# Kernel tuning notes

Measured on AMD Instinct MI355X. Metric: run time of the kernel, lower is better.

## Reference

```python
import jax, jax.numpy as jnp
import numpy as np

S, B, E = 2048, 2, 1024   # seq, batch, hidden (transpose_batch_sequence=True -> [S,B,E])
H, D = 16, 64             # num_heads, head_dim; H*D == E
EPS = 1e-6


def setup_inputs() -> dict:
    key = jax.random.key(0)
    k1, k2, k3 = jax.random.split(key, 3)
    x = jax.random.normal(k1, (S, B, E), dtype=jnp.float32)
    ln_scale = jnp.ones((E,), dtype=jnp.float32)
    # variance-scaling fan_in init ~ N(0, 1/fan_in); query block scaled by 1/sqrt(head_dim)
    w_qkv = jax.random.normal(k2, (E, 3 * H * D), dtype=jnp.float32) / np.sqrt(E)
    w_qkv = w_qkv.at[:, : H * D].divide(np.sqrt(D))  # scaled_query_init
    w_out = jax.random.normal(k3, (H * D, E), dtype=jnp.float32) / np.sqrt(H * D)
    return {"x": x, "ln_scale": ln_scale, "w_qkv": w_qkv, "w_out": w_out}


def reference(x, ln_scale, w_qkv, w_out):
    # LayerNormDenseGeneral: layernorm (scale only) fused with QKV projection
    mu = jnp.mean(x, axis=-1, keepdims=True)
    var = jnp.mean(jnp.square(x - mu), axis=-1, keepdims=True)
    ln = (x - mu) * jax.lax.rsqrt(var + EPS) * ln_scale          # [S,B,E]
    qkv = jnp.einsum('sbe,ef->sbf', ln, w_qkv)                    # [S,B,3HD]
    q, k, v = jnp.split(qkv, 3, axis=-1)
    q = q.reshape(S, B, H, D)
    k = k.reshape(S, B, H, D)
    v = v.reshape(S, B, H, D)
    # core_attention (transpose_batch_sequence=True): full score matrix
    attn = jnp.einsum('qbhd,kbhd->bhqk', q, k)                    # [B,H,S,S]
    attn = jax.nn.softmax(attn, axis=-1)
    ctx = jnp.einsum('bhqk,kbhd->qbhd', attn, v)                  # [S,B,H,D]
    ctx = ctx.reshape(S, B, H * D)
    out = jnp.einsum('sbf,fe->sbe', ctx, w_out)                   # output projection
    return out
```

## Files before the change

### kernel.cpp

```cpp
#include <hip/hip_runtime.h>
#include <math.h>


typedef unsigned short u16;
typedef unsigned int u32;
typedef __bf16 bf16x8 __attribute__((ext_vector_type(8)));
typedef float f32x4 __attribute__((ext_vector_type(4)));
typedef u16 u16x8 __attribute__((ext_vector_type(8)));
typedef u16 u16x4 __attribute__((ext_vector_type(4)));
typedef u32 u32x2 __attribute__((ext_vector_type(2)));

#define S_LEN 2048
#define BATCH 2
#define EDIM  1024
#define NHEAD 16
#define DHEAD 64
#define MROWS 4096
#define NQKV  3072
#define KDIM  1024
#define LOG2E 1.4426950408889634f

__device__ __forceinline__ float bf2f(u16 u) {
  union { unsigned int u; float f; } v; v.u = ((unsigned int)u) << 16; return v.f;
}
__device__ __forceinline__ u16 f2bf(float f) {
  union { float f; unsigned int u; } v; v.f = f;
  return (u16)((v.u + 0x7FFFu + ((v.u >> 16) & 1u)) >> 16);
}
__device__ __forceinline__ u32 cvt_pk_bf16(float lo, float hi) {
  u32 r;
  asm("v_cvt_pk_bf16_f32 %0, %1, %2" : "=v"(r) : "v"(lo), "v"(hi));
  return r;
}
__device__ __forceinline__ void glds16(const void* g, void* l) {
  __builtin_amdgcn_global_load_lds((__attribute__((address_space(1))) void*)g,
                                   (__attribute__((address_space(3))) void*)l,
                                   16, 0, 0);
}

__global__ void detect_kernel(const u16* __restrict__ x, int* __restrict__ flag) {
  const int t = threadIdx.x;
  const u16 v = x[t];
  const int e = (v >> 7) & 0xFF;
  const int ok = (e >= 100 && e <= 140) ? 1 : 0;
  const unsigned long long m = __ballot(ok);
  if (t == 0) *flag = (__popcll(m) >= 56) ? 1 : 0;
}

__global__ __launch_bounds__(256) void ln_kernel(const void* __restrict__ xv,
                                                 const void* __restrict__ scv,
                                                 u16* __restrict__ out,
                                                 const int* __restrict__ flag) {
  const int row = blockIdx.x;
  const int t = threadIdx.x;
  const int isbf = *flag;
  float v0, v1, v2, v3;
  if (isbf) {
    u16x4 xin = *(const u16x4*)((const u16*)xv + (size_t)row * EDIM + t * 4);
    v0 = bf2f(xin[0]); v1 = bf2f(xin[1]); v2 = bf2f(xin[2]); v3 = bf2f(xin[3]);
  } else {
    float4 xin = *(const float4*)((const float*)xv + (size_t)row * EDIM + t * 4);
    v0 = xin.x; v1 = xin.y; v2 = xin.z; v3 = xin.w;
  }
  float s  = v0 + v1 + v2 + v3;
  float ss = v0 * v0 + v1 * v1 + v2 * v2 + v3 * v3;
  #pragma unroll
  for (int off = 1; off < 64; off <<= 1) {
    s  += __shfl_xor(s, off);
    ss += __shfl_xor(ss, off);
  }
  __shared__ float ps[4], pq[4];
  const int w = t >> 6;
  if ((t & 63) == 0) { ps[w] = s; pq[w] = ss; }
  __syncthreads();
  s  = ps[0] + ps[1] + ps[2] + ps[3];
  ss = pq[0] + pq[1] + pq[2] + pq[3];
  const float mu   = s * (1.0f / EDIM);
  const float rstd = rsqrtf(ss * (1.0f / EDIM) - mu * mu + 1e-6f);
  float sc0, sc1, sc2, sc3;
  if (isbf) {
    const u16* sc = (const u16*)scv + t * 4;
    sc0 = bf2f(sc[0]); sc1 = bf2f(sc[1]); sc2 = bf2f(sc[2]); sc3 = bf2f(sc[3]);
  } else {
    const float* sc = (const float*)scv + t * 4;
    sc0 = sc[0]; sc1 = sc[1]; sc2 = sc[2]; sc3 = sc[3];
  }
  u16x4 o;
  o[0] = f2bf((v0 - mu) * rstd * sc0);
  o[1] = f2bf((v1 - mu) * rstd * sc1);
  o[2] = f2bf((v2 - mu) * rstd * sc2);
  o[3] = f2bf((v3 - mu) * rstd * sc3);
  *(u16x4*)(out + (size_t)row * EDIM + t * 4) = o;
}

__global__ __launch_bounds__(256) void transpose_cast(const void* __restrict__ inv,
                                                      u16* __restrict__ out,
                                                      int R, int C, int scaleCols,
                                                      const int* __restrict__ flag) {
  __shared__ u16 tile[32][33];
  const int isbf = *flag;
  const int tx = threadIdx.x, ty = threadIdx.y;
  const int c0 = blockIdx.x * 32, r0 = blockIdx.y * 32;
  const float scale = (c0 + tx < scaleCols) ? LOG2E : 1.0f;
  #pragma unroll
  for (int i = 0; i < 4; ++i) {
    const int r = r0 + ty + i * 8;
    float fv;
    if (isbf) fv = bf2f(((const u16*)inv)[(size_t)r * C + c0 + tx]);
    else      fv = ((const float*)inv)[(size_t)r * C + c0 + tx];
    tile[ty + i * 8][tx] = f2bf(fv * scale);
  }
  __syncthreads();
  #pragma unroll
  for (int i = 0; i < 4; ++i)
    out[(size_t)(c0 + ty + i * 8) * R + r0 + tx] = tile[tx][ty + i * 8];
}

template <int OUT_F32>
__global__ __launch_bounds__(256) void gemm_bt(const u16* __restrict__ A,
                                               const u16* __restrict__ Bt,
                                               void* __restrict__ Cv,
                                               const int N) {
  __shared__ __align__(16) u16 As[2][128][32];
  __shared__ __align__(16) u16 Bs[2][128][32];
  const int t = threadIdx.x;
  const int w = t >> 6, lane = t & 63;
  const int quad = lane >> 4, l16 = lane & 15;
  const int bn = blockIdx.x * 128, bm = blockIdx.y * 128;
  const int wm = (w >> 1) * 64, wn = (w & 1) * 64;
  const int arow = lane >> 2, aseg = (lane & 3) * 8;
  f32x4 acc[4][4] = {};
  const u16* Ab = A  + (size_t)(bm + arow) * KDIM + aseg;
  const u16* Bb = Bt + (size_t)(bn + arow) * KDIM + aseg;
  #pragma unroll
  for (int i = 0; i < 2; ++i) {
    const int rb = w * 32 + i * 16;
    glds16(Ab + (size_t)rb * KDIM, &As[0][rb][0]);
    glds16(Bb + (size_t)rb * KDIM, &Bs[0][rb][0]);
  }
  __syncthreads();
  int cur = 0;
  for (int kt = 0; kt < KDIM; kt += 32) {
    if (kt + 32 < KDIM) {
      #pragma unroll
      for (int i = 0; i < 2; ++i) {
        const int rb = w * 32 + i * 16;
        glds16(Ab + (size_t)rb * KDIM + kt + 32, &As[cur ^ 1][rb][0]);
        glds16(Bb + (size_t)rb * KDIM + kt + 32, &Bs[cur ^ 1][rb][0]);
      }
    }
    bf16x8 af[4], bfv[4];
    #pragma unroll
    for (int mt = 0; mt < 4; ++mt) af[mt]  = *(const bf16x8*)&As[cur][wm + mt * 16 + l16][quad * 8];
    #pragma unroll
    for (int nt = 0; nt < 4; ++nt) bfv[nt] = *(const bf16x8*)&Bs[cur][wn + nt * 16 + l16][quad * 8];
    #pragma unroll
    for (int mt = 0; mt < 4; ++mt)
      #pragma unroll
      for (int nt = 0; nt < 4; ++nt)
        acc[mt][nt] = __builtin_amdgcn_mfma_f32_16x16x32_bf16(af[mt], bfv[nt], acc[mt][nt], 0, 0, 0);
    __syncthreads();
    cur ^= 1;
  }
  #pragma unroll
  for (int mt = 0; mt < 4; ++mt)
    #pragma unroll
    for (int nt = 0; nt < 4; ++nt)
      #pragma unroll
      for (int r = 0; r < 4; ++r) {
        const int row = bm + wm + mt * 16 + quad * 4 + r;
        const int col = bn + wn + nt * 16 + l16;
        if (OUT_F32) ((float*)Cv)[(size_t)row * N + col] = acc[mt][nt][r];
        else         ((u16*)Cv)[(size_t)row * N + col] = f2bf(acc[mt][nt][r]);
      }
}

__global__ __launch_bounds__(256) void vtrans_kernel(const u16* __restrict__ qkv,
                                                     u16* __restrict__ vT) {
  __shared__ u16 tile[64][65];
  const int t = threadIdx.x;
  const int s0 = blockIdx.x * 64;
  const int bh = blockIdx.y, b = bh >> 4, h = bh & 15;
  const u16* src = qkv + 2 * EDIM + h * DHEAD;
  #pragma unroll
  for (int i = 0; i < 16; ++i) {
    const int idx = i * 256 + t;
    const int sl = idx >> 6, d = idx & 63;
    tile[sl][d] = src[(size_t)((s0 + sl) * 2 + b) * NQKV + d];
  }
  __syncthreads();
  u16* dst = vT + (size_t)bh * DHEAD * S_LEN + s0;
  #pragma unroll
  for (int i = 0; i < 16; ++i) {
    const int idx = i * 256 + t;
    const int dr = idx >> 6, sl = idx & 63;
    dst[(size_t)dr * S_LEN + sl] = tile[sl][dr];
  }
}

__global__ __launch_bounds__(256) void attn_kernel(const u16* __restrict__ qkv,
                                                   const u16* __restrict__ vT,
                                                   u16* __restrict__ ctx) {
  __shared__ __align__(16) u16 Ks[2][64][64];
  __shared__ __align__(16) u16 Vs[2][64][64];
  __shared__ __align__(16) u16 Ps[64][64];
  const int t = threadIdx.x;
  const int w = t >> 6, lane = t & 63;
  const int quad = lane >> 4, l16 = lane & 15;
  const int q0 = blockIdx.x * 64;
  const int bh = blockIdx.y, b = bh >> 4, h = bh & 15;
  const u16* qbase = qkv + h * DHEAD;
  const u16* kbase = qkv + EDIM + h * DHEAD;
  const u16* vbase = vT + (size_t)bh * DHEAD * S_LEN;

  bf16x8 qf[2];
  #pragma unroll
  for (int ks = 0; ks < 2; ++ks)
    qf[ks] = *(const bf16x8*)(qbase + (size_t)((q0 + w * 16 + l16) * 2 + b) * NQKV + ks * 32 + quad * 8);

  const int srow = lane >> 3;
  const int schk = (lane & 7) ^ srow;
  const int rdswz = (l16 & 7);
  const int pswz = (l16 & 7) * 2;

  bf16x8 onesf;
  #pragma unroll
  for (int j = 0; j < 8; ++j) onesf[j] = (__bf16)1.0f;

  f32x4 oacc[4] = {};
  f32x4 sacc = {};

  #pragma unroll
  for (int i = 0; i < 2; ++i) {
    const int rb = (w * 2 + i) * 8;
    const int row = rb + srow;
    glds16(kbase + (size_t)(row * 2 + b) * NQKV + schk * 8, &Ks[0][rb][0]);
    glds16(vbase + (size_t)row * S_LEN + schk * 8, &Vs[0][rb][0]);
  }
  __syncthreads();

  for (int kc = 0; kc < S_LEN / 64; ++kc) {
    const int nb = kc & 1;
    if (kc + 1 < S_LEN / 64) {
      #pragma unroll
      for (int i = 0; i < 2; ++i) {
        const int rb = (w * 2 + i) * 8;
        const int row = rb + srow;
        glds16(kbase + (size_t)(((kc + 1) * 64 + row) * 2 + b) * NQKV + schk * 8, &Ks[nb ^ 1][rb][0]);
        glds16(vbase + (size_t)row * S_LEN + (kc + 1) * 64 + schk * 8, &Vs[nb ^ 1][rb][0]);
      }
    }
    bf16x8 kf[4][2];
    #pragma unroll
    for (int nt = 0; nt < 4; ++nt)
      #pragma unroll
      for (int ks = 0; ks < 2; ++ks)
        kf[nt][ks] = *(const bf16x8*)&Ks[nb][nt * 16 + l16][((ks * 4 + quad) ^ rdswz) * 8];
    f32x4 sa[4] = {};
    #pragma unroll
    for (int ks = 0; ks < 2; ++ks)
      #pragma unroll
      for (int nt = 0; nt < 4; ++nt)
        sa[nt] = __builtin_amdgcn_mfma_f32_16x16x32_bf16(kf[nt][ks], qf[ks], sa[nt], 0, 0, 0);
    #pragma unroll
    for (int nt = 0; nt < 4; ++nt) {
      const float p0 = exp2f(sa[nt][0]);
      const float p1 = exp2f(sa[nt][1]);
      const float p2 = exp2f(sa[nt][2]);
      const float p3 = exp2f(sa[nt][3]);
      u32x2 pw;
      pw[0] = cvt_pk_bf16(p0, p1);
      pw[1] = cvt_pk_bf16(p2, p3);
      *(u32x2*)&Ps[w * 16 + l16][(((nt * 4 + quad) ^ pswz) & 15) * 4] = pw;
    }
    bf16x8 vf[4][2];
    #pragma unroll
    for (int nd = 0; nd < 4; ++nd)
      #pragma unroll
      for (int ks = 0; ks < 2; ++ks)
        vf[nd][ks] = *(const bf16x8*)&Vs[nb][nd * 16 + l16][((ks * 4 + quad) ^ rdswz) * 8];
    asm volatile("s_waitcnt lgkmcnt(0)" ::: "memory");
    __builtin_amdgcn_sched_barrier(0);
    bf16x8 pf0 = *(const bf16x8*)&Ps[w * 16 + l16][(((quad * 2) ^ pswz) & 15) * 4];
    bf16x8 pf1 = *(const bf16x8*)&Ps[w * 16 + l16][(((8 + quad * 2) ^ pswz) & 15) * 4];
    #pragma unroll
    for (int nd = 0; nd < 4; ++nd) {
      oacc[nd] = __builtin_amdgcn_mfma_f32_16x16x32_bf16(pf0, vf[nd][0], oacc[nd], 0, 0, 0);
      oacc[nd] = __builtin_amdgcn_mfma_f32_16x16x32_bf16(pf1, vf[nd][1], oacc[nd], 0, 0, 0);
    }
    sacc = __builtin_amdgcn_mfma_f32_16x16x32_bf16(pf0, onesf, sacc, 0, 0, 0);
    sacc = __builtin_amdgcn_mfma_f32_16x16x32_bf16(pf1, onesf, sacc, 0, 0, 0);
    __syncthreads();
  }
  #pragma unroll
  for (int r = 0; r < 4; ++r) {
    const float inv = 1.0f / sacc[r];
    const int srowq = q0 + w * 16 + quad * 4 + r;
    #pragma unroll
    for (int nd = 0; nd < 4; ++nd) {
      const int col = h * DHEAD + nd * 16 + l16;
      ctx[(size_t)(srowq * 2 + b) * EDIM + col] = f2bf(oacc[nd][r] * inv);
    }
  }
}

extern "C" void kernel_launch(void* const* d_in, const int* in_sizes, int n_in,
                              void* d_out, int out_size, void* d_ws, size_t ws_size,
                              hipStream_t stream) {
  const void* x = nullptr; const void* sc = nullptr;
  const void* wq = nullptr; const void* wo = nullptr;
  for (int i = 0; i < n_in; ++i) {
    switch (in_sizes[i]) {
      case 4194304: x  = d_in[i]; break;
      case 1024:    sc = d_in[i]; break;
      case 3145728: wq = d_in[i]; break;
      case 1048576: wo = d_in[i]; break;
      default: break;
    }
  }
  if (!x)  x  = d_in[0];
  if (!sc) sc = d_in[1];
  if (!wq) wq = d_in[2];
  if (!wo) wo = d_in[3];

  char* ws = (char*)d_ws;
  u16* lnb   = (u16*)(ws);
  u16* wqkvT = (u16*)(ws + 8388608);
  u16* woutT = (u16*)(ws + 14680064);
  u16* qkv   = (u16*)(ws + 16777216);
  u16* vT    = (u16*)(ws + 41943040);
  u16* ctx   = (u16*)(ws + 50331648);
  int* flag  = (int*)(ws + 58720256);

  detect_kernel<<<1, 64, 0, stream>>>((const u16*)x, flag);
  ln_kernel<<<MROWS, 256, 0, stream>>>(x, sc, lnb, flag);
  transpose_cast<<<dim3(NQKV / 32, KDIM / 32), dim3(32, 8), 0, stream>>>(wq, wqkvT, KDIM, NQKV, 1024, flag);
  transpose_cast<<<dim3(EDIM / 32, EDIM / 32), dim3(32, 8), 0, stream>>>(wo, woutT, EDIM, EDIM, 0, flag);
  gemm_bt<0><<<dim3(NQKV / 128, MROWS / 128), 256, 0, stream>>>(lnb, wqkvT, qkv, NQKV);
  vtrans_kernel<<<dim3(S_LEN / 64, BATCH * NHEAD), 256, 0, stream>>>(qkv, vT);
  attn_kernel<<<dim3(S_LEN / 64, BATCH * NHEAD), 256, 0, stream>>>(qkv, vT, ctx);
  gemm_bt<1><<<dim3(EDIM / 128, MROWS / 128), 256, 0, stream>>>(ctx, woutT, d_out, EDIM);
}
```

Baseline: 213.1 us.

## Merge prep kernels into one launch and fuse V transpose into QKV GEMM epilogue

```diff
diff --git a/kernel.cpp b/kernel.cpp
--- a/kernel.cpp
+++ b/kernel.cpp
@@ -8,6 +8,7 @@
 typedef float f32x4 __attribute__((ext_vector_type(4)));
 typedef u16 u16x8 __attribute__((ext_vector_type(8)));
 typedef u16 u16x4 __attribute__((ext_vector_type(4)));
+typedef u16 u16x2 __attribute__((ext_vector_type(2)));
 typedef u32 u32x2 __attribute__((ext_vector_type(2)));
 
 #define S_LEN 2048
@@ -38,91 +39,97 @@
                                    16, 0, 0);
 }
 
-__global__ void detect_kernel(const u16* __restrict__ x, int* __restrict__ flag) {
+__global__ __launch_bounds__(256) void prep_kernel(const void* __restrict__ xv,
+                                                   const void* __restrict__ scv,
+                                                   const void* __restrict__ wqv,
+                                                   const void* __restrict__ wov,
+                                                   u16* __restrict__ lnb,
+                                                   u16* __restrict__ wqkvT,
+                                                   u16* __restrict__ woutT) {
   const int t = threadIdx.x;
-  const u16 v = x[t];
-  const int e = (v >> 7) & 0xFF;
-  const int ok = (e >= 100 && e <= 140) ? 1 : 0;
-  const unsigned long long m = __ballot(ok);
-  if (t == 0) *flag = (__popcll(m) >= 56) ? 1 : 0;
-}
-
-__global__ __launch_bounds__(256) void ln_kernel(const void* __restrict__ xv,
-                                                 const void* __restrict__ scv,
-                                                 u16* __restrict__ out,
-                                                 const int* __restrict__ flag) {
-  const int row = blockIdx.x;
-  const int t = threadIdx.x;
-  const int isbf = *flag;
-  float v0, v1, v2, v3;
-  if (isbf) {
-    u16x4 xin = *(const u16x4*)((const u16*)xv + (size_t)row * EDIM + t * 4);
-    v0 = bf2f(xin[0]); v1 = bf2f(xin[1]); v2 = bf2f(xin[2]); v3 = bf2f(xin[3]);
+  const u16 dv = ((const u16*)xv)[t & 63];
+  const int de = (dv >> 7) & 0xFF;
+  const unsigned long long dm = __ballot(de >= 100 && de <= 140);
+  const int isbf = (__popcll(dm) >= 56) ? 1 : 0;
+  const int bid = blockIdx.x;
+
+  if (bid < MROWS) {
+    const int row = bid;
+    float v0, v1, v2, v3;
+    if (isbf) {
+      u16x4 xin = *(const u16x4*)((const u16*)xv + (size_t)row * EDIM + t * 4);
+      v0 = bf2f(xin[0]); v1 = bf2f(xin[1]); v2 = bf2f(xin[2]); v3 = bf2f(xin[3]);
+    } else {
+      float4 xin = *(const float4*)((const float*)xv + (size_t)row * EDIM + t * 4);
+      v0 = xin.x; v1 = xin.y; v2 = xin.z; v3 = xin.w;
+    }
+    float s  = v0 + v1 + v2 + v3;
+    float ss = v0 * v0 + v1 * v1 + v2 * v2 + v3 * v3;
+    #pragma unroll
+    for (int off = 1; off < 64; off <<= 1) {
+      s  += __shfl_xor(s, off);
+      ss += __shfl_xor(ss, off);
+    }
+    __shared__ float ps[4], pq[4];
+    const int w = t >> 6;
+    if ((t & 63) == 0) { ps[w] = s; pq[w] = ss; }
+    __syncthreads();
+    s  = ps[0] + ps[1] + ps[2] + ps[3];
+    ss = pq[0] + pq[1] + pq[2] + pq[3];
+    const float mu   = s * (1.0f / EDIM);
+    const float rstd = rsqrtf(ss * (1.0f / EDIM) - mu * mu + 1e-6f);
+    float sc0, sc1, sc2, sc3;
+    if (isbf) {
+      const u16* sc = (const u16*)scv + t * 4;
+      sc0 = bf2f(sc[0]); sc1 = bf2f(sc[1]); sc2 = bf2f(sc[2]); sc3 = bf2f(sc[3]);
+    } else {
+      const float* sc = (const float*)scv + t * 4;
+      sc0 = sc[0]; sc1 = sc[1]; sc2 = sc[2]; sc3 = sc[3];
+    }
+    u16x4 o;
+    o[0] = f2bf((v0 - mu) * rstd * sc0);
+    o[1] = f2bf((v1 - mu) * rstd * sc1);
+    o[2] = f2bf((v2 - mu) * rstd * sc2);
+    o[3] = f2bf((v3 - mu) * rstd * sc3);
+    *(u16x4*)(lnb + (size_t)row * EDIM + t * 4) = o;
   } else {
-    float4 xin = *(const float4*)((const float*)xv + (size_t)row * EDIM + t * 4);
-    v0 = xin.x; v1 = xin.y; v2 = xin.z; v3 = xin.w;
-  }
-  float s  = v0 + v1 + v2 + v3;
-  float ss = v0 * v0 + v1 * v1 + v2 * v2 + v3 * v3;
-  #pragma unroll
-  for (int off = 1; off < 64; off <<= 1) {
-    s  += __shfl_xor(s, off);
-    ss += __shfl_xor(ss, off);
-  }
-  __shared__ float ps[4], pq[4];
-  const int w = t >> 6;
-  if ((t & 63) == 0) { ps[w] = s; pq[w] = ss; }
-  __syncthreads();
-  s  = ps[0] + ps[1] + ps[2] + ps[3];
-  ss = pq[0] + pq[1] + pq[2] + pq[3];
-  const float mu   = s * (1.0f / EDIM);
-  const float rstd = rsqrtf(ss * (1.0f / EDIM) - mu * mu + 1e-6f);
-  float sc0, sc1, sc2, sc3;
-  if (isbf) {
-    const u16* sc = (const u16*)scv + t * 4;
-    sc0 = bf2f(sc[0]); sc1 = bf2f(sc[1]); sc2 = bf2f(sc[2]); sc3 = bf2f(sc[3]);
-  } else {
-    const float* sc = (const float*)scv + t * 4;
-    sc0 = sc[0]; sc1 = sc[1]; sc2 = sc[2]; sc3 = sc[3];
-  }
-  u16x4 o;
-  o[0] = f2bf((v0 - mu) * rstd * sc0);
-  o[1] = f2bf((v1 - mu) * rstd * sc1);
-  o[2] = f2bf((v2 - mu) * rstd * sc2);
-  o[3] = f2bf((v3 - mu) * rstd * sc3);
-  *(u16x4*)(out + (size_t)row * EDIM + t * 4) = o;
-}
-
-__global__ __launch_bounds__(256) void transpose_cast(const void* __restrict__ inv,
-                                                      u16* __restrict__ out,
-                                                      int R, int C, int scaleCols,
-                                                      const int* __restrict__ flag) {
-  __shared__ u16 tile[32][33];
-  const int isbf = *flag;
-  const int tx = threadIdx.x, ty = threadIdx.y;
-  const int c0 = blockIdx.x * 32, r0 = blockIdx.y * 32;
-  const float scale = (c0 + tx < scaleCols) ? LOG2E : 1.0f;
-  #pragma unroll
-  for (int i = 0; i < 4; ++i) {
-    const int r = r0 + ty + i * 8;
-    float fv;
-    if (isbf) fv = bf2f(((const u16*)inv)[(size_t)r * C + c0 + tx]);
-    else      fv = ((const float*)inv)[(size_t)r * C + c0 + tx];
-    tile[ty + i * 8][tx] = f2bf(fv * scale);
-  }
-  __syncthreads();
-  #pragma unroll
-  for (int i = 0; i < 4; ++i)
-    out[(size_t)(c0 + ty + i * 8) * R + r0 + tx] = tile[tx][ty + i * 8];
-}
-
-template <int OUT_F32>
+    __shared__ u16 tile[32][33];
+    int gx, gy, R, C, scaleCols;
+    const void* inv; u16* out;
+    if (bid < MROWS + 3072) {
+      const int idx = bid - MROWS;
+      gx = idx % 96; gy = idx / 96;
+      R = KDIM; C = NQKV; scaleCols = 1024; inv = wqv; out = wqkvT;
+    } else {
+      const int idx = bid - MROWS - 3072;
+      gx = idx & 31; gy = idx >> 5;
+      R = EDIM; C = EDIM; scaleCols = 0; inv = wov; out = woutT;
+    }
+    const int tx = t & 31, ty = t >> 5;
+    const int c0 = gx * 32, r0 = gy * 32;
+    const float scale = (c0 + tx < scaleCols) ? LOG2E : 1.0f;
+    #pragma unroll
+    for (int i = 0; i < 4; ++i) {
+      const int r = r0 + ty + i * 8;
+      float fv;
+      if (isbf) fv = bf2f(((const u16*)inv)[(size_t)r * C + c0 + tx]);
+      else      fv = ((const float*)inv)[(size_t)r * C + c0 + tx];
+      tile[ty + i * 8][tx] = f2bf(fv * scale);
+    }
+    __syncthreads();
+    #pragma unroll
+    for (int i = 0; i < 4; ++i)
+      out[(size_t)(c0 + ty + i * 8) * R + r0 + tx] = tile[tx][ty + i * 8];
+  }
+}
+
+template <int OUT_F32, int V_EP>
 __global__ __launch_bounds__(256) void gemm_bt(const u16* __restrict__ A,
                                                const u16* __restrict__ Bt,
                                                void* __restrict__ Cv,
-                                               const int N) {
-  __shared__ __align__(16) u16 As[2][128][32];
-  __shared__ __align__(16) u16 Bs[2][128][32];
+                                               const int N,
+                                               u16* __restrict__ vT) {
+  __shared__ __align__(16) u16 pool[2][2][128][32];
   const int t = threadIdx.x;
   const int w = t >> 6, lane = t & 63;
   const int quad = lane >> 4, l16 = lane & 15;
@@ -135,8 +142,8 @@
   #pragma unroll
   for (int i = 0; i < 2; ++i) {
     const int rb = w * 32 + i * 16;
-    glds16(Ab + (size_t)rb * KDIM, &As[0][rb][0]);
-    glds16(Bb + (size_t)rb * KDIM, &Bs[0][rb][0]);
+    glds16(Ab + (size_t)rb * KDIM, &pool[0][0][rb][0]);
+    glds16(Bb + (size_t)rb * KDIM, &pool[1][0][rb][0]);
   }
   __syncthreads();
   int cur = 0;
@@ -145,15 +152,15 @@
       #pragma unroll
       for (int i = 0; i < 2; ++i) {
         const int rb = w * 32 + i * 16;
-        glds16(Ab + (size_t)rb * KDIM + kt + 32, &As[cur ^ 1][rb][0]);
-        glds16(Bb + (size_t)rb * KDIM + kt + 32, &Bs[cur ^ 1][rb][0]);
+        glds16(Ab + (size_t)rb * KDIM + kt + 32, &pool[0][cur ^ 1][rb][0]);
+        glds16(Bb + (size_t)rb * KDIM + kt + 32, &pool[1][cur ^ 1][rb][0]);
       }
     }
     bf16x8 af[4], bfv[4];
     #pragma unroll
-    for (int mt = 0; mt < 4; ++mt) af[mt]  = *(const bf16x8*)&As[cur][wm + mt * 16 + l16][quad * 8];
-    #pragma unroll
-    for (int nt = 0; nt < 4; ++nt) bfv[nt] = *(const bf16x8*)&Bs[cur][wn + nt * 16 + l16][quad * 8];
+    for (int mt = 0; mt < 4; ++mt) af[mt]  = *(const bf16x8*)&pool[0][cur][wm + mt * 16 + l16][quad * 8];
+    #pragma unroll
+    for (int nt = 0; nt < 4; ++nt) bfv[nt] = *(const bf16x8*)&pool[1][cur][wn + nt * 16 + l16][quad * 8];
     #pragma unroll
     for (int mt = 0; mt < 4; ++mt)
       #pragma unroll
@@ -162,6 +169,40 @@
     __syncthreads();
     cur ^= 1;
   }
+
+  if (V_EP && bn >= 2048) {
+    u16* scr = &pool[0][0][0][0];
+    #pragma unroll
+    for (int mt = 0; mt < 4; ++mt)
+      #pragma unroll
+      for (int nt = 0; nt < 4; ++nt) {
+        const int col = wn + nt * 16 + l16;
+        const int hh = col >> 6, dd = col & 63;
+        const int unit = (wm >> 2) + mt * 4 + quad;
+        const int up = (((unit >> 2) ^ (dd & 7)) << 2) + (unit & 3);
+        const int base = (hh * 64 + dd) * 128;
+        u16x2 e0, e1;
+        e0[0] = f2bf(acc[mt][nt][0]); e0[1] = f2bf(acc[mt][nt][2]);
+        e1[0] = f2bf(acc[mt][nt][1]); e1[1] = f2bf(acc[mt][nt][3]);
+        *(u16x2*)&scr[base + up * 2]      = e0;
+        *(u16x2*)&scr[base + 64 + up * 2] = e1;
+      }
+    __syncthreads();
+    const int s0 = bm >> 1;
+    const int hbase = (bn - 2048) >> 6;
+    #pragma unroll
+    for (int i = 0; i < 8; ++i) {
+      const int cid = i * 256 + t;
+      const int u4 = cid & 7;
+      const int b  = (cid >> 3) & 1;
+      const int dd = (cid >> 4) & 63;
+      const int hh = cid >> 10;
+      const u16x8 val = *(const u16x8*)&scr[(hh * 64 + dd) * 128 + b * 64 + ((u4 ^ (dd & 7)) << 3)];
+      *(u16x8*)&vT[(size_t)((b * 16 + hbase + hh) * 64 + dd) * S_LEN + s0 + u4 * 8] = val;
+    }
+    return;
+  }
+
   #pragma unroll
   for (int mt = 0; mt < 4; ++mt)
     #pragma unroll
@@ -173,29 +214,6 @@
         if (OUT_F32) ((float*)Cv)[(size_t)row * N + col] = acc[mt][nt][r];
         else         ((u16*)Cv)[(size_t)row * N + col] = f2bf(acc[mt][nt][r]);
       }
-}
-
-__global__ __launch_bounds__(256) void vtrans_kernel(const u16* __restrict__ qkv,
-                                                     u16* __restrict__ vT) {
-  __shared__ u16 tile[64][65];
-  const int t = threadIdx.x;
-  const int s0 = blockIdx.x * 64;
-  const int bh = blockIdx.y, b = bh >> 4, h = bh & 15;
-  const u16* src = qkv + 2 * EDIM + h * DHEAD;
-  #pragma unroll
-  for (int i = 0; i < 16; ++i) {
-    const int idx = i * 256 + t;
-    const int sl = idx >> 6, d = idx & 63;
-    tile[sl][d] = src[(size_t)((s0 + sl) * 2 + b) * NQKV + d];
-  }
-  __syncthreads();
-  u16* dst = vT + (size_t)bh * DHEAD * S_LEN + s0;
-  #pragma unroll
-  for (int i = 0; i < 16; ++i) {
-    const int idx = i * 256 + t;
-    const int dr = idx >> 6, sl = idx & 63;
-    dst[(size_t)dr * S_LEN + sl] = tile[sl][dr];
-  }
 }
 
 __global__ __launch_bounds__(256) void attn_kernel(const u16* __restrict__ qkv,
@@ -330,14 +348,9 @@
   u16* qkv   = (u16*)(ws + 16777216);
   u16* vT    = (u16*)(ws + 41943040);
   u16* ctx   = (u16*)(ws + 50331648);
-  int* flag  = (int*)(ws + 58720256);
-
-  detect_kernel<<<1, 64, 0, stream>>>((const u16*)x, flag);
-  ln_kernel<<<MROWS, 256, 0, stream>>>(x, sc, lnb, flag);
-  transpose_cast<<<dim3(NQKV / 32, KDIM / 32), dim3(32, 8), 0, stream>>>(wq, wqkvT, KDIM, NQKV, 1024, flag);
-  transpose_cast<<<dim3(EDIM / 32, EDIM / 32), dim3(32, 8), 0, stream>>>(wo, woutT, EDIM, EDIM, 0, flag);
-  gemm_bt<0><<<dim3(NQKV / 128, MROWS / 128), 256, 0, stream>>>(lnb, wqkvT, qkv, NQKV);
-  vtrans_kernel<<<dim3(S_LEN / 64, BATCH * NHEAD), 256, 0, stream>>>(qkv, vT);
+
+  prep_kernel<<<MROWS + 3072 + 1024, 256, 0, stream>>>(x, sc, wq, wo, lnb, wqkvT, woutT);
+  gemm_bt<0, 1><<<dim3(NQKV / 128, MROWS / 128), 256, 0, stream>>>(lnb, wqkvT, qkv, NQKV, vT);
   attn_kernel<<<dim3(S_LEN / 64, BATCH * NHEAD), 256, 0, stream>>>(qkv, vT, ctx);
-  gemm_bt<1><<<dim3(EDIM / 128, MROWS / 128), 256, 0, stream>>>(ctx, woutT, d_out, EDIM);
-}
+  gemm_bt<1, 0><<<dim3(EDIM / 128, MROWS / 128), 256, 0, stream>>>(ctx, woutT, d_out, EDIM, nullptr);
+}
```

Result: faster. 202.0 us (-5.2%).
